# Performance work log

Measured on AMD Instinct MI355X. Metric: run time of the kernel, lower is better.

## Reference

```python
import jax, jax.numpy as jnp
import numpy as np

N_OBJ, N_EVT, N_EDGE, N_MAIN = 50000, 100000, 500000, 25000
OBJ_DIM, EVT_DIM = 256, 256


def setup_inputs() -> dict:
    key = jax.random.key(0)
    ks = jax.random.split(key, 12)
    s = 1.0 / np.sqrt(OBJ_DIM)
    return {
        "object_X": jax.random.normal(ks[0], (N_OBJ, OBJ_DIM), jnp.float32),
        "event_X": jax.random.normal(ks[1], (N_EVT, EVT_DIM), jnp.float32),
        "lc_obj_idx": jax.random.randint(ks[2], (N_EDGE,), 0, N_OBJ),
        "lc_evt_idx": jax.random.randint(ks[3], (N_EDGE,), 0, N_EVT),
        "main_idx": jax.random.randint(ks[4], (N_MAIN,), 0, N_OBJ),
        # lifecycle_proj: Linear(event_dim, obj_dim)
        "W_proj": jax.random.uniform(ks[5], (OBJ_DIM, EVT_DIM), jnp.float32, -s, s),
        "b_proj": jax.random.uniform(ks[6], (OBJ_DIM,), jnp.float32, -s, s),
        # GRUCell(obj_dim, obj_dim): weight_ih/hh are [3*H, H]
        "W_ih": jax.random.uniform(ks[7], (3 * OBJ_DIM, OBJ_DIM), jnp.float32, -s, s),
        "b_ih": jax.random.uniform(ks[8], (3 * OBJ_DIM,), jnp.float32, -s, s),
        "W_hh": jax.random.uniform(ks[9], (3 * OBJ_DIM, OBJ_DIM), jnp.float32, -s, s),
        "b_hh": jax.random.uniform(ks[10], (3 * OBJ_DIM,), jnp.float32, -s, s),
    }


def reference(object_X, event_X, lc_obj_idx, lc_evt_idx, main_idx,
              W_proj, b_proj, W_ih, b_ih, W_hh, b_hh):
    n_obj = object_X.shape[0]
    # gather event feats, linear + ReLU  -> [E, obj_dim]
    proj = jax.nn.relu(event_X[lc_evt_idx] @ W_proj.T + b_proj)
    # scatter_mean over target objects (empty slots -> 0, like torch_scatter)
    sums = jax.ops.segment_sum(proj, lc_obj_idx, num_segments=n_obj)
    cnt = jax.ops.segment_sum(jnp.ones((lc_obj_idx.shape[0],), proj.dtype),
                              lc_obj_idx, num_segments=n_obj)
    profile = sums / jnp.maximum(cnt, 1.0)[:, None]  # [N_obj, obj_dim]
    # GRUCell(profile, object_X)
    gi = profile @ W_ih.T + b_ih   # [N_obj, 3H]
    gh = object_X @ W_hh.T + b_hh  # [N_obj, 3H]
    i_r, i_z, i_n = jnp.split(gi, 3, axis=-1)
    h_r, h_z, h_n = jnp.split(gh, 3, axis=-1)
    r = jax.nn.sigmoid(i_r + h_r)
    z = jax.nn.sigmoid(i_z + h_z)
    n = jnp.tanh(i_n + r * h_n)
    updated = (1.0 - z) * n + z * object_X
    # masked blend: only main objects take updated values
    mask = jnp.zeros((n_obj, 1), object_X.dtype).at[main_idx].set(1.0)
    return mask * updated + (1.0 - mask) * object_X
```

## Files before the change

kernel.cpp:

```cpp
#include <hip/hip_runtime.h>

typedef unsigned short u16;
typedef __attribute__((ext_vector_type(8))) short bf16x8;
typedef __attribute__((ext_vector_type(4))) float f32x4;

struct __align__(8) u16x4_t { u16 x, y, z, w; };

__device__ __forceinline__ float b2f(u16 b) {
  union { unsigned u; float f; } v; v.u = ((unsigned)b) << 16; return v.f;
}
__device__ __forceinline__ u16 f2b(float f) {
  union { float f; unsigned u; } v; v.f = f;
  unsigned r = v.u + 0x7fffu + ((v.u >> 16) & 1u);
  return (u16)(r >> 16);
}
__device__ __forceinline__ unsigned pk2(float lo, float hi) {
  unsigned r;
  asm("v_cvt_pk_bf16_f32 %0, %1, %2" : "=v"(r) : "v"(lo), "v"(hi));
  return r;
}

__global__ void prep(const float* __restrict__ Wp, const float* __restrict__ Wi,
                     const float* __restrict__ Wh, u16* __restrict__ wb,
                     const int* __restrict__ main_idx, int* __restrict__ mask,
                     int* __restrict__ mlist, int* __restrict__ cpos,
                     int* __restrict__ mcount, int nMain) {
  int b = blockIdx.x;
  if (b < 448) {
    int t = b * 256 + threadIdx.x;
    const float* src; int o;
    if (t < 16384)      { src = Wp; o = t; }
    else if (t < 65536) { src = Wi; o = t - 16384; }
    else                { src = Wh; o = t - 65536; }
    float4 v = ((const float4*)src)[o];
    u16x4_t q;
    q.x = f2b(v.x); q.y = f2b(v.y); q.z = f2b(v.z); q.w = f2b(v.w);
    ((u16x4_t*)wb)[t] = q;
  } else {
    int t = (b - 448) * 256 + threadIdx.x;
    if (t < nMain) {
      int o = main_idx[t];
      if (atomicCAS(&mask[o], 0, 1) == 0) {
        int i = atomicAdd(mcount, 1);
        mlist[i] = o;
        cpos[o] = i;
      }
    }
  }
}

__global__ void count_edges(const int* __restrict__ obj_idx, const int* __restrict__ mask,
                            int* __restrict__ deg, int n) {
  int e = blockIdx.x * 256 + threadIdx.x;
  if (e >= n) return;
  int o = obj_idx[e];
  if (mask[o]) atomicAdd(&deg[o], 1);
}

__global__ __launch_bounds__(256)
void alloc_offs(const int* __restrict__ mlist, const int* __restrict__ mcount,
                const int* __restrict__ deg, int* __restrict__ offs,
                int* __restrict__ tcur, int* __restrict__ rrows, int Mpad) {
  int i = blockIdx.x * 256 + threadIdx.x;
  int lane = threadIdx.x & 63;
  int mc = *mcount;
  if (i < Mpad) rrows[i] = (i < mc) ? mlist[i] : 0;
  int o = (i < mc) ? mlist[i] : 0;
  int d = (i < mc) ? deg[o] : 0;
  int x = d;
#pragma unroll
  for (int s = 1; s < 64; s <<= 1) {
    int y = __shfl_up(x, s, 64);
    if (lane >= s) x += y;
  }
  int wt = __shfl(x, 63, 64);
  int base = 0;
  if (lane == 63 && wt > 0) base = atomicAdd(tcur, wt);
  base = __shfl(base, 63, 64);
  if (i < mc) offs[o] = base + (x - d);
}

__global__ void fill_edges(const int* __restrict__ obj_idx, const int* __restrict__ evt_idx,
                           const int* __restrict__ mask, const int* __restrict__ offs,
                           int* __restrict__ cursor, int* __restrict__ elist, int n) {
  int e = blockIdx.x * 256 + threadIdx.x;
  if (e >= n) return;
  int o = obj_idx[e];
  if (!mask[o]) return;
  int pos = atomicAdd(&cursor[o], 1);
  elist[offs[o] + pos] = evt_idx[e];
}

__global__ __launch_bounds__(256)
void accum_gather(const u16* __restrict__ P, const int* __restrict__ elist,
                  const int* __restrict__ offs, const int* __restrict__ deg,
                  const int* __restrict__ mlist, const int* __restrict__ mcount,
                  const float* __restrict__ objX, const int* __restrict__ rrows,
                  u16* __restrict__ prof, u16* __restrict__ objc, int Mpad) {
  const int wave = threadIdx.x >> 6;
  const int lane = threadIdx.x & 63;
  const int i = blockIdx.x * 4 + wave;
  if (i >= Mpad) return;

  int src = rrows[i];
  float4 xv = *(const float4*)(objX + (size_t)src * 256 + lane * 4);

  const int mc = *mcount;
  float a0 = 0.f, a1 = 0.f, a2 = 0.f, a3 = 0.f;
  int d = 0;
  if (i < mc) {
    const int o = mlist[i];
    const int off = offs[o];
    d = deg[o];
    int j = 0;
    for (; j + 1 < d; j += 2) {
      int e0 = elist[off + j], e1 = elist[off + j + 1];
      u16x4_t p0 = *(const u16x4_t*)(P + (size_t)e0 * 256 + lane * 4);
      u16x4_t p1 = *(const u16x4_t*)(P + (size_t)e1 * 256 + lane * 4);
      a0 += b2f(p0.x) + b2f(p1.x);
      a1 += b2f(p0.y) + b2f(p1.y);
      a2 += b2f(p0.z) + b2f(p1.z);
      a3 += b2f(p0.w) + b2f(p1.w);
    }
    if (j < d) {
      int e0 = elist[off + j];
      u16x4_t p0 = *(const u16x4_t*)(P + (size_t)e0 * 256 + lane * 4);
      a0 += b2f(p0.x); a1 += b2f(p0.y); a2 += b2f(p0.z); a3 += b2f(p0.w);
    }
  }
  float s = 1.f / fmaxf((float)d, 1.f);
  u16x4_t pv;
  pv.x = f2b(a0 * s); pv.y = f2b(a1 * s); pv.z = f2b(a2 * s); pv.w = f2b(a3 * s);
  *(u16x4_t*)(prof + (size_t)i * 256 + lane * 4) = pv;

  u16x4_t ov;
  ov.x = f2b(xv.x); ov.y = f2b(xv.y); ov.z = f2b(xv.z); ov.w = f2b(xv.w);
  *(u16x4_t*)(objc + (size_t)i * 256 + lane * 4) = ov;
}

template<int RELU>
__device__ __forceinline__
void gemm_core(const u16* __restrict__ A, const u16* __restrict__ B,
               const float* __restrict__ bias, u16* __restrict__ C,
               int M, int N, int n0, int m0, u16* lA, u16* lB) {
  const int tid  = threadIdx.x;
  const int lane = tid & 63;
  const int wave = tid >> 6;
  const int mR = (wave & 1) * 64;
  const int nC = (wave >> 1) * 64;

  int srow[4], skq[4];
#pragma unroll
  for (int s = 0; s < 4; ++s) {
    int g = s * 256 + tid;
    srow[s] = g >> 3;
    skq[s]  = ((g & 7) ^ ((g >> 3) & 7)) << 3;
  }

  f32x4 acc[4][4] = {};

  auto STAGE = [&](int buf, int kt) {
#pragma unroll
    for (int s = 0; s < 4; ++s) {
      int row = srow[s];
      int ar = m0 + row; ar = (ar < M) ? ar : (M - 1);
      const u16* gA = A + (size_t)ar * 256 + kt + skq[s];
      __builtin_amdgcn_global_load_lds(
          (const __attribute__((address_space(1))) void*)gA,
          (__attribute__((address_space(3))) void*)(lA + buf * 8192 + s * 2048 + wave * 512),
          16, 0, 0);
      const u16* gB = B + (size_t)(n0 + row) * 256 + kt + skq[s];
      __builtin_amdgcn_global_load_lds(
          (const __attribute__((address_space(1))) void*)gB,
          (__attribute__((address_space(3))) void*)(lB + buf * 8192 + s * 2048 + wave * 512),
          16, 0, 0);
    }
  };

  STAGE(0, 0);
  __syncthreads();

  for (int t = 0; t < 4; ++t) {
    const int cur = t & 1;
    if (t < 3) STAGE(cur ^ 1, (t + 1) * 64);
    const u16* bA = lA + cur * 8192;
    const u16* bB = lB + cur * 8192;
#pragma unroll
    for (int ks = 0; ks < 2; ++ks) {
      const int kbq = ks * 4 + (lane >> 4);
      bf16x8 af[4], bf[4];
#pragma unroll
      for (int i = 0; i < 4; ++i) {
        int ra = mR + i * 16 + (lane & 15);
        af[i] = *(const bf16x8*)(bA + ra * 64 + ((kbq ^ (ra & 7)) << 3));
        int rb = nC + i * 16 + (lane & 15);
        bf[i] = *(const bf16x8*)(bB + rb * 64 + ((kbq ^ (rb & 7)) << 3));
      }
#pragma unroll
      for (int i = 0; i < 4; ++i)
#pragma unroll
        for (int j = 0; j < 4; ++j)
          acc[i][j] = __builtin_amdgcn_mfma_f32_16x16x32_bf16(af[i], bf[j], acc[i][j], 0, 0, 0);
    }
    __syncthreads();
  }

  const int crow = (lane >> 4) * 4;
  const int ccol = lane & 15;
#pragma unroll
  for (int i = 0; i < 4; ++i) {
#pragma unroll
    for (int j = 0; j < 4; ++j) {
      int col = n0 + nC + j * 16 + ccol;
      float bv = bias[col];
#pragma unroll
      for (int q = 0; q < 4; ++q) {
        int row = m0 + mR + i * 16 + crow + q;
        if (row < M) {
          float v = acc[i][j][q] + bv;
          if (RELU) v = fmaxf(v, 0.f);
          C[(size_t)row * N + col] = f2b(v);
        }
      }
    }
  }
}

__device__ __forceinline__ int xcd_swz(int bid, int nwg) {
  int q = nwg >> 3, r = nwg & 7;
  int xcd = bid & 7, loc = bid >> 3;
  return (xcd < r ? xcd * (q + 1) : r * (q + 1) + (xcd - r) * q) + loc;
}

__global__ __launch_bounds__(256, 2)
void gemm_pf(const float* __restrict__ A, const u16* __restrict__ B,
             const float* __restrict__ bias, u16* __restrict__ C, int M, int nwg) {
  __shared__ u16 lA[2 * 8192];
  __shared__ u16 lB[2 * 8192];
  int wg = xcd_swz(blockIdx.x, nwg);
  const int n0 = (wg & 1) * 128;
  const int m0 = (wg >> 1) * 128;

  const int tid  = threadIdx.x;
  const int lane = tid & 63;
  const int wave = tid >> 6;
  const int mR = (wave & 1) * 64;
  const int nC = (wave >> 1) * 64;

  const float* aptr[4];
  int sdst[4], skq[4], srow[4];
#pragma unroll
  for (int s = 0; s < 4; ++s) {
    int g = s * 256 + tid;
    int row = g >> 3, q = g & 7;
    srow[s] = row;
    sdst[s] = row * 64 + ((q ^ (row & 7)) << 3);
    skq[s]  = (q ^ (row & 7)) << 3;
    int ar = m0 + row; ar = (ar < M) ? ar : (M - 1);
    aptr[s] = A + (size_t)ar * 256 + q * 8;
  }

  f32x4 acc[4][4] = {};
  float4 fa[4][2];

  auto LOAD_A = [&](int kt) {
#pragma unroll
    for (int s = 0; s < 4; ++s) {
      fa[s][0] = *(const float4*)(aptr[s] + kt);
      fa[s][1] = *(const float4*)(aptr[s] + kt + 4);
    }
  };
  auto WRITE_A = [&](int buf) {
#pragma unroll
    for (int s = 0; s < 4; ++s) {
      uint4 w;
      w.x = pk2(fa[s][0].x, fa[s][0].y);
      w.y = pk2(fa[s][0].z, fa[s][0].w);
      w.z = pk2(fa[s][1].x, fa[s][1].y);
      w.w = pk2(fa[s][1].z, fa[s][1].w);
      *(uint4*)(lA + buf * 8192 + sdst[s]) = w;
    }
  };
  auto STAGE_B = [&](int buf, int kt) {
#pragma unroll
    for (int s = 0; s < 4; ++s) {
      const u16* gB = B + (size_t)(n0 + srow[s]) * 256 + kt + skq[s];
      __builtin_amdgcn_global_load_lds(
          (const __attribute__((address_space(1))) void*)gB,
          (__attribute__((address_space(3))) void*)(lB + buf * 8192 + s * 2048 + wave * 512),
          16, 0, 0);
    }
  };

  LOAD_A(0); STAGE_B(0, 0);
  WRITE_A(0);
  __syncthreads();

  for (int t = 0; t < 4; ++t) {
    const int cur = t & 1;
    if (t < 3) { LOAD_A((t + 1) * 64); STAGE_B(cur ^ 1, (t + 1) * 64); }
    const u16* bA = lA + cur * 8192;
    const u16* bB = lB + cur * 8192;
#pragma unroll
    for (int ks = 0; ks < 2; ++ks) {
      const int kbq = ks * 4 + (lane >> 4);
      bf16x8 af[4], bf[4];
#pragma unroll
      for (int i = 0; i < 4; ++i) {
        int ra = mR + i * 16 + (lane & 15);
        af[i] = *(const bf16x8*)(bA + ra * 64 + ((kbq ^ (ra & 7)) << 3));
        int rb = nC + i * 16 + (lane & 15);
        bf[i] = *(const bf16x8*)(bB + rb * 64 + ((kbq ^ (rb & 7)) << 3));
      }
#pragma unroll
      for (int i = 0; i < 4; ++i)
#pragma unroll
        for (int j = 0; j < 4; ++j)
          acc[i][j] = __builtin_amdgcn_mfma_f32_16x16x32_bf16(af[i], bf[j], acc[i][j], 0, 0, 0);
    }
    if (t < 3) WRITE_A(cur ^ 1);
    __syncthreads();
  }

  const int crow = (lane >> 4) * 4;
  const int ccol = lane & 15;
#pragma unroll
  for (int i = 0; i < 4; ++i) {
#pragma unroll
    for (int j = 0; j < 4; ++j) {
      int col = n0 + nC + j * 16 + ccol;
      float bv = bias[col];
#pragma unroll
      for (int q = 0; q < 4; ++q) {
        int row = m0 + mR + i * 16 + crow + q;
        if (row < M) {
          float v = acc[i][j][q] + bv;
          C[(size_t)row * 256 + col] = f2b(fmaxf(v, 0.f));
        }
      }
    }
  }
}

__global__ __launch_bounds__(256, 2)
void gemm2_dual(const u16* __restrict__ prof, const u16* __restrict__ objc,
                const u16* __restrict__ wib, const u16* __restrict__ whb,
                const float* __restrict__ bi, const float* __restrict__ bh,
                u16* __restrict__ gi, u16* __restrict__ gh, int Mpad, int nwg) {
  __shared__ u16 lA[2 * 8192];
  __shared__ u16 lB[2 * 8192];
  int wg = xcd_swz(blockIdx.x, nwg);
  int m0 = (wg / 12) * 128;
  int y = wg % 12;
  if (y < 6) gemm_core<0>(prof, wib, bi, gi, Mpad, 768, y * 128, m0, lA, lB);
  else       gemm_core<0>(objc, whb, bh, gh, Mpad, 768, (y - 6) * 128, m0, lA, lB);
}

__global__ __launch_bounds__(256)
void gate_out(const u16* __restrict__ gi, const u16* __restrict__ gh,
              const float* __restrict__ objX, const int* __restrict__ mask,
              const int* __restrict__ cpos, float* __restrict__ out, int nObj) {
  const int wave = threadIdx.x >> 6;
  const int lane = threadIdx.x & 63;
  const int row = blockIdx.x * 4 + wave;
  if (row >= nObj) return;
  float4 x4 = *(const float4*)(objX + (size_t)row * 256 + lane * 4);
  float4 r4 = x4;
  if (mask[row]) {
    size_t b = (size_t)cpos[row] * 768 + lane * 4;
    u16x4_t ir = *(const u16x4_t*)(gi + b);
    u16x4_t iz = *(const u16x4_t*)(gi + b + 256);
    u16x4_t in_ = *(const u16x4_t*)(gi + b + 512);
    u16x4_t hr = *(const u16x4_t*)(gh + b);
    u16x4_t hz = *(const u16x4_t*)(gh + b + 256);
    u16x4_t hn = *(const u16x4_t*)(gh + b + 512);
    float xs[4] = {x4.x, x4.y, x4.z, x4.w};
    u16 irs[4] = {ir.x, ir.y, ir.z, ir.w};
    u16 izs[4] = {iz.x, iz.y, iz.z, iz.w};
    u16 ins[4] = {in_.x, in_.y, in_.z, in_.w};
    u16 hrs[4] = {hr.x, hr.y, hr.z, hr.w};
    u16 hzs[4] = {hz.x, hz.y, hz.z, hz.w};
    u16 hns[4] = {hn.x, hn.y, hn.z, hn.w};
    float rs[4];
#pragma unroll
    for (int q = 0; q < 4; ++q) {
      float r = 1.f / (1.f + __expf(-(b2f(irs[q]) + b2f(hrs[q]))));
      float z = 1.f / (1.f + __expf(-(b2f(izs[q]) + b2f(hzs[q]))));
      float a = b2f(ins[q]) + r * b2f(hns[q]);
      float n = 1.f - 2.f / (__expf(2.f * a) + 1.f);
      rs[q] = (1.f - z) * n + z * xs[q];
    }
    r4.x = rs[0]; r4.y = rs[1]; r4.z = rs[2]; r4.w = rs[3];
  }
  *(float4*)(out + (size_t)row * 256 + lane * 4) = r4;
}


extern "C" void kernel_launch(void* const* d_in, const int* in_sizes, int n_in,
                              void* d_out, int out_size, void* d_ws, size_t ws_size,
                              hipStream_t stream) {
  const float* objX   = (const float*)d_in[0];
  const float* evtX   = (const float*)d_in[1];
  const int* obj_idx  = (const int*)d_in[2];
  const int* evt_idx  = (const int*)d_in[3];
  const int* main_idx = (const int*)d_in[4];
  const float* Wp = (const float*)d_in[5];
  const float* bp = (const float*)d_in[6];
  const float* Wi = (const float*)d_in[7];
  const float* bi = (const float*)d_in[8];
  const float* Wh = (const float*)d_in[9];
  const float* bh = (const float*)d_in[10];

  const int nObj  = in_sizes[0] / 256;
  const int nEvt  = in_sizes[1] / 256;
  const int nEdge = in_sizes[2];
  const int nMain = in_sizes[4];
  const int Mpad  = ((nMain + 127) / 128) * 128;

  char* ws = (char*)d_ws;
  u16*   P     = (u16*)(ws + 0);
  u16*   gi    = (u16*)(ws + 0);
  u16*   gh    = (u16*)(ws + 51200000);
  u16*   prof  = (u16*)(ws + 89735168);
  u16*   objc  = (u16*)(ws + 102580224);
  u16*   wb    = (u16*)(ws + 166625280);
  u16*   wpb   = wb;
  u16*   wib   = wb + 65536;
  u16*   whb   = wb + 262144;
  int*   deg   = (int*)(ws + 167542784);
  int*   cursor= (int*)(ws + 167742784);
  int*   mask  = (int*)(ws + 167942784);
  int*   mcount= (int*)(ws + 168142784);
  int*   tcur  = (int*)(ws + 168142848);
  int*   cpos  = (int*)(ws + 168142912);
  int*   offs  = (int*)(ws + 168342912);
  int*   mlist = (int*)(ws + 168542912);
  int*   rrows = (int*)(ws + 168643264);
  int*   elist = (int*)(ws + 168743616);
  float* out   = (float*)d_out;

  hipMemsetAsync(ws + 167542784, 0, 600128, stream);

  const int prepGrid = 448 + (nMain + 255) / 256;
  prep<<<prepGrid, 256, 0, stream>>>(Wp, Wi, Wh, wb,
                                     main_idx, mask, mlist, cpos, mcount, nMain);

  const int nwgP = ((nEvt + 127) / 128) * 2;
  gemm_pf<<<nwgP, 256, 0, stream>>>(evtX, wpb, bp, P, nEvt, nwgP);

  count_edges<<<(nEdge + 255) / 256, 256, 0, stream>>>(obj_idx, mask, deg, nEdge);
  alloc_offs<<<Mpad / 256, 256, 0, stream>>>(mlist, mcount, deg, offs, tcur, rrows, Mpad);
  fill_edges<<<(nEdge + 255) / 256, 256, 0, stream>>>(obj_idx, evt_idx, mask, offs, cursor, elist, nEdge);

  accum_gather<<<(Mpad + 3) / 4, 256, 0, stream>>>(P, elist, offs, deg, mlist, mcount,
                                                   objX, rrows, prof, objc, Mpad);

  const int nwg = (Mpad / 128) * 12;
  gemm2_dual<<<nwg, 256, 0, stream>>>(prof, objc, wib, whb, bi, bh, gi, gh, Mpad, nwg);

  gate_out<<<(nObj + 3) / 4, 256, 0, stream>>>(gi, gh, objX, mask, cpos, out, nObj);
}
```

Before: 379.7 us.

## Load full-width N tile per block and stage fp32 A directly to LDS

The event projection GEMM now uses one 512-thread block per 128-row M tile covering all 256 output columns. Each fp32 row of the gathered event matrix is therefore read from global memory once instead of by two blocks. A is copied to LDS in fp32 through async global_load_lds and converted to bf16 when fragments are read, which replaces the register round-trip and pack step. K is processed in 32-wide steps with a new swizzled layout. The trade-offs are twice the LDS bytes for A, more conversion work per fragment, and more barriers.

Result: faster. 372.2 us (-2.0%).

```diff
diff --git a/kernel.cpp b/kernel.cpp
--- a/kernel.cpp
+++ b/kernel.cpp
@@ -232,93 +232,80 @@
   return (xcd < r ? xcd * (q + 1) : r * (q + 1) + (xcd - r) * q) + loc;
 }
 
-__global__ __launch_bounds__(256, 2)
+__global__ __launch_bounds__(512, 2)
 void gemm_pf(const float* __restrict__ A, const u16* __restrict__ B,
-             const float* __restrict__ bias, u16* __restrict__ C, int M, int nwg) {
-  __shared__ u16 lA[2 * 8192];
-  __shared__ u16 lB[2 * 8192];
-  int wg = xcd_swz(blockIdx.x, nwg);
-  const int n0 = (wg & 1) * 128;
-  const int m0 = (wg >> 1) * 128;
-
+             const float* __restrict__ bias, u16* __restrict__ C, int M) {
+  __shared__ float lA[2][128 * 32];
+  __shared__ u16   lB[2][128 * 64];
   const int tid  = threadIdx.x;
   const int lane = tid & 63;
   const int wave = tid >> 6;
+  const int m0 = blockIdx.x * 128;
   const int mR = (wave & 1) * 64;
   const int nC = (wave >> 1) * 64;
 
-  const float* aptr[4];
-  int sdst[4], skq[4], srow[4];
-#pragma unroll
-  for (int s = 0; s < 4; ++s) {
-    int g = s * 256 + tid;
-    int row = g >> 3, q = g & 7;
-    srow[s] = row;
-    sdst[s] = row * 64 + ((q ^ (row & 7)) << 3);
-    skq[s]  = (q ^ (row & 7)) << 3;
+  const float* asrc[2];
+  const u16*   bsrc[2];
+#pragma unroll
+  for (int s = 0; s < 2; ++s) {
+    int g = s * 512 + tid;
+    int row = g >> 3, qp = g & 7;
+    int q = qp ^ (row & 7);
     int ar = m0 + row; ar = (ar < M) ? ar : (M - 1);
-    aptr[s] = A + (size_t)ar * 256 + q * 8;
-  }
+    asrc[s] = A + (size_t)ar * 256 + q * 4;
+    int bq = qp ^ (row & 7);
+    int n  = row * 2 + (bq >> 2);
+    bsrc[s] = B + (size_t)n * 256 + (bq & 3) * 8;
+  }
+
+  auto STAGE = [&](int buf, int kt) {
+#pragma unroll
+    for (int s = 0; s < 2; ++s) {
+      int g = s * 512 + tid;
+      __builtin_amdgcn_global_load_lds(
+          (const __attribute__((address_space(1))) void*)(asrc[s] + kt),
+          (__attribute__((address_space(3))) void*)(&lA[buf][g * 4]),
+          16, 0, 0);
+      __builtin_amdgcn_global_load_lds(
+          (const __attribute__((address_space(1))) void*)(bsrc[s] + kt),
+          (__attribute__((address_space(3))) void*)(&lB[buf][g * 8]),
+          16, 0, 0);
+    }
+  };
 
   f32x4 acc[4][4] = {};
-  float4 fa[4][2];
-
-  auto LOAD_A = [&](int kt) {
-#pragma unroll
-    for (int s = 0; s < 4; ++s) {
-      fa[s][0] = *(const float4*)(aptr[s] + kt);
-      fa[s][1] = *(const float4*)(aptr[s] + kt + 4);
-    }
-  };
-  auto WRITE_A = [&](int buf) {
-#pragma unroll
-    for (int s = 0; s < 4; ++s) {
-      uint4 w;
-      w.x = pk2(fa[s][0].x, fa[s][0].y);
-      w.y = pk2(fa[s][0].z, fa[s][0].w);
-      w.z = pk2(fa[s][1].x, fa[s][1].y);
-      w.w = pk2(fa[s][1].z, fa[s][1].w);
-      *(uint4*)(lA + buf * 8192 + sdst[s]) = w;
-    }
-  };
-  auto STAGE_B = [&](int buf, int kt) {
-#pragma unroll
-    for (int s = 0; s < 4; ++s) {
-      const u16* gB = B + (size_t)(n0 + srow[s]) * 256 + kt + skq[s];
-      __builtin_amdgcn_global_load_lds(
-          (const __attribute__((address_space(1))) void*)gB,
-          (__attribute__((address_space(3))) void*)(lB + buf * 8192 + s * 2048 + wave * 512),
-          16, 0, 0);
-    }
-  };
-
-  LOAD_A(0); STAGE_B(0, 0);
-  WRITE_A(0);
+  STAGE(0, 0);
   __syncthreads();
 
-  for (int t = 0; t < 4; ++t) {
+  const int h = lane >> 4;
+  for (int t = 0; t < 8; ++t) {
     const int cur = t & 1;
-    if (t < 3) { LOAD_A((t + 1) * 64); STAGE_B(cur ^ 1, (t + 1) * 64); }
-    const u16* bA = lA + cur * 8192;
-    const u16* bB = lB + cur * 8192;
-#pragma unroll
-    for (int ks = 0; ks < 2; ++ks) {
-      const int kbq = ks * 4 + (lane >> 4);
-      bf16x8 af[4], bf[4];
-#pragma unroll
-      for (int i = 0; i < 4; ++i) {
-        int ra = mR + i * 16 + (lane & 15);
-        af[i] = *(const bf16x8*)(bA + ra * 64 + ((kbq ^ (ra & 7)) << 3));
-        int rb = nC + i * 16 + (lane & 15);
-        bf[i] = *(const bf16x8*)(bB + rb * 64 + ((kbq ^ (rb & 7)) << 3));
-      }
-#pragma unroll
-      for (int i = 0; i < 4; ++i)
-#pragma unroll
-        for (int j = 0; j < 4; ++j)
-          acc[i][j] = __builtin_amdgcn_mfma_f32_16x16x32_bf16(af[i], bf[j], acc[i][j], 0, 0, 0);
-    }
-    if (t < 3) WRITE_A(cur ^ 1);
+    if (t < 7) STAGE(cur ^ 1, (t + 1) * 32);
+    const float* bA = lA[cur];
+    const u16*   bB = lB[cur];
+    bf16x8 af[4], bf[4];
+#pragma unroll
+    for (int i = 0; i < 4; ++i) {
+      int ra = mR + i * 16 + (lane & 15);
+      int pg = (2 * h) ^ (ra & 7);
+      float4 x = *(const float4*)(bA + ra * 32 + pg * 4);
+      float4 y = *(const float4*)(bA + ra * 32 + (pg ^ 1) * 4);
+      union { unsigned u[4]; bf16x8 v; } cv;
+      cv.u[0] = pk2(x.x, x.y); cv.u[1] = pk2(x.z, x.w);
+      cv.u[2] = pk2(y.x, y.y); cv.u[3] = pk2(y.z, y.w);
+      af[i] = cv.v;
+    }
+#pragma unroll
+    for (int j = 0; j < 4; ++j) {
+      int rb = nC + j * 16 + (lane & 15);
+      int qp = (((rb & 1) << 2) | h) ^ ((rb >> 1) & 7);
+      bf[j] = *(const bf16x8*)(bB + (rb >> 1) * 64 + qp * 8);
+    }
+#pragma unroll
+    for (int i = 0; i < 4; ++i)
+#pragma unroll
+      for (int j = 0; j < 4; ++j)
+        acc[i][j] = __builtin_amdgcn_mfma_f32_16x16x32_bf16(af[i], bf[j], acc[i][j], 0, 0, 0);
     __syncthreads();
   }
 
@@ -328,15 +315,13 @@
   for (int i = 0; i < 4; ++i) {
 #pragma unroll
     for (int j = 0; j < 4; ++j) {
-      int col = n0 + nC + j * 16 + ccol;
+      int col = nC + j * 16 + ccol;
       float bv = bias[col];
 #pragma unroll
       for (int q = 0; q < 4; ++q) {
         int row = m0 + mR + i * 16 + crow + q;
-        if (row < M) {
-          float v = acc[i][j][q] + bv;
-          C[(size_t)row * 256 + col] = f2b(fmaxf(v, 0.f));
-        }
+        if (row < M)
+          C[(size_t)row * 256 + col] = f2b(fmaxf(acc[i][j][q] + bv, 0.f));
       }
     }
   }
@@ -445,8 +430,7 @@
   prep<<<prepGrid, 256, 0, stream>>>(Wp, Wi, Wh, wb,
                                      main_idx, mask, mlist, cpos, mcount, nMain);
 
-  const int nwgP = ((nEvt + 127) / 128) * 2;
-  gemm_pf<<<nwgP, 256, 0, stream>>>(evtX, wpb, bp, P, nEvt, nwgP);
+  gemm_pf<<<(nEvt + 127) / 128, 512, 0, stream>>>(evtX, wpb, bp, P, nEvt);
 
   count_edges<<<(nEdge + 255) / 256, 256, 0, stream>>>(obj_idx, mask, deg, nEdge);
   alloc_offs<<<Mpad / 256, 256, 0, stream>>>(mlist, mcount, deg, offs, tcur, rrows, Mpad);
```
